# Kernel optimization log

Hardware: AMD Instinct MI355X
Metric: run time of the kernel (lower is better)

The kernel has to match this reference:

```python
import jax, jax.numpy as jnp
import numpy as np

INPUT_SIZE = 256
HIDDEN = 512

def setup_inputs() -> dict:
    key = jax.random.key(0)
    ks = jax.random.split(key, 12)
    B, T, I, H = 64, 1024, INPUT_SIZE, HIDDEN
    s = 1.0 / np.sqrt(I + H)
    x = jax.random.normal(ks[0], (B, T, I), dtype=jnp.float32)
    Wf = jax.random.uniform(ks[1], (I + H, H), jnp.float32, -s, s)
    bf = jax.random.uniform(ks[2], (H,), jnp.float32, -s, s)
    Wi = jax.random.uniform(ks[3], (I + H, H), jnp.float32, -s, s)
    bi = jax.random.uniform(ks[4], (H,), jnp.float32, -s, s)
    Wc = jax.random.uniform(ks[5], (I + H, H), jnp.float32, -s, s)
    bc = jax.random.uniform(ks[6], (H,), jnp.float32, -s, s)
    Wo = jax.random.uniform(ks[7], (I + H, H), jnp.float32, -s, s)
    bo = jax.random.uniform(ks[8], (H,), jnp.float32, -s, s)
    sf = 1.0 / np.sqrt(H)
    W_fc = jax.random.uniform(ks[9], (H, 1), jnp.float32, -sf, sf)
    b_fc = jax.random.uniform(ks[10], (1,), jnp.float32, -sf, sf)
    return {"x": x, "Wf": Wf, "bf": bf, "Wi": Wi, "bi": bi,
            "Wc": Wc, "bc": bc, "Wo": Wo, "bo": bo,
            "W_fc": W_fc, "b_fc": b_fc}

def reference(x, Wf, bf, Wi, bi, Wc, bc, Wo, bo, W_fc, b_fc):
    B, T, I = x.shape
    H = Wf.shape[1]
    # Fuse the 4 gate GEMMs into one [I+H, 4H] matmul (same math, one launch).
    W = jnp.concatenate([Wf, Wi, Wc, Wo], axis=1)   # [I+H, 4H]
    b = jnp.concatenate([bf, bi, bc, bo], axis=0)   # [4H]
    h0 = jnp.zeros((B, H), x.dtype)
    c0 = jnp.zeros((B, H), x.dtype)

    def step(carry, xt):
        h, c = carry
        combined = jnp.concatenate([xt, h], axis=1)     # [B, I+H]
        gates = combined @ W + b                        # [B, 4H]
        f, i, c_tilde, o = jnp.split(gates, 4, axis=1)
        f = jax.nn.sigmoid(f)
        i = jax.nn.sigmoid(i)
        c_tilde = jnp.tanh(c_tilde)
        o = jax.nn.sigmoid(o)
        c = f * c + i * c_tilde
        h = o * jnp.tanh(c)
        return (h, c), None

    (h, c), _ = jax.lax.scan(step, (h0, c0), jnp.swapaxes(x, 0, 1))
    return h @ W_fc + b_fc  # [B, 1]
```

## Files before the change

### kernel.cpp

```cpp
#include <hip/hip_runtime.h>
#include <hip/hip_fp16.h>


#define T_STEPS 1024
#define BATCH   64
#define ISZ     256
#define HSZ     512
#define NWG     128
#define NTHR    256
#define HB4     ((BATCH * HSZ) / 4)

typedef _Float16 half8  __attribute__((ext_vector_type(8)));
typedef _Float16 half4  __attribute__((ext_vector_type(4)));
typedef float    floatx4 __attribute__((ext_vector_type(4)));
typedef unsigned long long u64;

#define LD_AGENT(p)     __hip_atomic_load((p), __ATOMIC_RELAXED, __HIP_MEMORY_SCOPE_AGENT)
#define ST_AGENT(p, v)  __hip_atomic_store((p), (v), __ATOMIC_RELAXED, __HIP_MEMORY_SCOPE_AGENT)
#define ADD_AGENT(p, v) __hip_atomic_fetch_add((p), (v), __ATOMIC_RELAXED, __HIP_MEMORY_SCOPE_AGENT)

__device__ __forceinline__ float fast_sigmoid(float x) {
    return 1.0f / (1.0f + __expf(-x));
}
__device__ __forceinline__ float fast_tanh(float x) {
    return 1.0f - 2.0f / (__expf(2.0f * x) + 1.0f);
}

__global__ __launch_bounds__(NTHR, 1) void lstm_persist(
    const float* __restrict__ x,
    const float* __restrict__ Wf, const float* __restrict__ bfv,
    const float* __restrict__ Wi, const float* __restrict__ biv,
    const float* __restrict__ Wc, const float* __restrict__ bcv,
    const float* __restrict__ Wo, const float* __restrict__ bov,
    u64* __restrict__ hbuf4, unsigned* __restrict__ ctrs)
{
    const int g    = blockIdx.x;
    const int tid  = threadIdx.x;
    const int w    = tid >> 6;
    const int l    = tid & 63;
    const int lj   = l & 15;
    const int lk   = l >> 4;
    const int gate = lj >> 2;
    const int jc   = lj & 3;
    const int hc   = (g << 2) + jc;
    const int row0 = w << 4;
    const int arow = row0 + lj;
    const int grp  = g >> 3;

    const float* Wg = (gate == 0) ? Wf : (gate == 1) ? Wi : (gate == 2) ? Wc : Wo;
    const float* bg = (gate == 0) ? bfv : (gate == 1) ? biv : (gate == 2) ? bcv : bov;

    half8 Bfrag[24];
    #pragma unroll
    for (int kf = 0; kf < 24; ++kf) {
        half8 v;
        #pragma unroll
        for (int e = 0; e < 8; ++e) {
            int k = (kf << 5) + (lk << 3) + e;
            v[e] = (_Float16)Wg[(size_t)k * HSZ + hc];
        }
        Bfrag[kf] = v;
    }
    const float bias = bg[hc];
    float cst[4] = {0.f, 0.f, 0.f, 0.f};

    unsigned* lvl1 = &ctrs[grp * 16];
    unsigned* root = &ctrs[16 * 16];

    floatx4 accx = {0.f, 0.f, 0.f, 0.f};
    {
        const float* xr = x + (size_t)arow * T_STEPS * ISZ + (lk << 3);
        #pragma unroll
        for (int kf = 0; kf < 8; ++kf) {
            floatx4 x0 = *(const floatx4*)(xr + (kf << 5));
            floatx4 x1 = *(const floatx4*)(xr + (kf << 5) + 4);
            half8 a;
            a[0] = (_Float16)x0[0]; a[1] = (_Float16)x0[1];
            a[2] = (_Float16)x0[2]; a[3] = (_Float16)x0[3];
            a[4] = (_Float16)x1[0]; a[5] = (_Float16)x1[1];
            a[6] = (_Float16)x1[2]; a[7] = (_Float16)x1[3];
            accx = __builtin_amdgcn_mfma_f32_16x16x32_f16(a, Bfrag[kf], accx, 0, 0, 0);
        }
    }

    for (int t = 0; t < T_STEPS; ++t) {
        floatx4 acc;
        #pragma unroll
        for (int e = 0; e < 4; ++e) acc[e] = accx[e] + bias;

        if (t > 0) {
            if (tid == 0) {
                const unsigned tgt = 16u * (unsigned)t;
                while (LD_AGENT(root) < tgt) __builtin_amdgcn_s_sleep(1);
            }
            __syncthreads();

            const u64* hr = hbuf4 + (size_t)(t & 1) * HB4 + arow;
            u64 hl[32];
            #pragma unroll
            for (int kf = 0; kf < 16; ++kf) {
                const int c0 = kf * 8 + lk * 2;
                hl[2 * kf]     = LD_AGENT(hr + (size_t)c0 * BATCH);
                hl[2 * kf + 1] = LD_AGENT(hr + (size_t)(c0 + 1) * BATCH);
            }
            #pragma unroll
            for (int kf = 0; kf < 16; ++kf) {
                union { u64 u[2]; half8 h; } a;
                a.u[0] = hl[2 * kf];
                a.u[1] = hl[2 * kf + 1];
                acc = __builtin_amdgcn_mfma_f32_16x16x32_f16(a.h, Bfrag[8 + kf], acc, 0, 0, 0);
            }
        }

        floatx4 act;
        if (gate == 2) {
            #pragma unroll
            for (int e = 0; e < 4; ++e) act[e] = fast_tanh(acc[e]);
        } else {
            #pragma unroll
            for (int e = 0; e < 4; ++e) act[e] = fast_sigmoid(acc[e]);
        }

        const int base = l & ~12;
        float hv[4];
        #pragma unroll
        for (int e = 0; e < 4; ++e) {
            float vf = __shfl(act[e], base);
            float vi = __shfl(act[e], base + 4);
            float vc = __shfl(act[e], base + 8);
            float vo = __shfl(act[e], base + 12);
            float c  = vf * cst[e] + vi * vc;
            cst[e] = c;
            hv[e] = vo * fast_tanh(c);
        }

        half4 outv;
        #pragma unroll
        for (int col = 0; col < 4; ++col) {
            const int src = ((l & 15) >> 2) * 16 + col;
            float sel = 0.f;
            #pragma unroll
            for (int e = 0; e < 4; ++e) {
                float tmp = __shfl(hv[e], src);
                if ((l & 3) == e) sel = tmp;
            }
            outv[col] = (_Float16)sel;
        }
        u64* hw = hbuf4 + (size_t)((t + 1) & 1) * HB4 + (size_t)g * BATCH + row0;
        if (l < 16) {
            union { half4 h; u64 u; } pk; pk.h = outv;
            ST_AGENT(hw + l, pk.u);
        }
        asm volatile("s_waitcnt vmcnt(0)" ::: "memory");
        __syncthreads();

        if (tid == 0) {
            unsigned old = ADD_AGENT(lvl1, 1u);
            if (old == 8u * (unsigned)(t + 1) - 1u)
                ADD_AGENT(root, 1u);
        }

        if (t + 1 < T_STEPS) {
            floatx4 az = {0.f, 0.f, 0.f, 0.f};
            const float* xr = x + ((size_t)arow * T_STEPS + (t + 1)) * ISZ + (lk << 3);
            #pragma unroll
            for (int kf = 0; kf < 8; ++kf) {
                floatx4 x0 = *(const floatx4*)(xr + (kf << 5));
                floatx4 x1 = *(const floatx4*)(xr + (kf << 5) + 4);
                half8 a;
                a[0] = (_Float16)x0[0]; a[1] = (_Float16)x0[1];
                a[2] = (_Float16)x0[2]; a[3] = (_Float16)x0[3];
                a[4] = (_Float16)x1[0]; a[5] = (_Float16)x1[1];
                a[6] = (_Float16)x1[2]; a[7] = (_Float16)x1[3];
                az = __builtin_amdgcn_mfma_f32_16x16x32_f16(a, Bfrag[kf], az, 0, 0, 0);
            }
            accx = az;
        }
    }
}

__global__ void out_proj(const u64* __restrict__ hb4, const float* __restrict__ Wfc,
                         const float* __restrict__ bfc, float* __restrict__ out)
{
    const int b = blockIdx.x;
    const int l = threadIdx.x;
    float s = 0.f;
    #pragma unroll
    for (int j = 0; j < 2; ++j) {
        const int c4 = l + (j << 6);
        union { u64 u; half4 h; } v;
        v.u = hb4[(size_t)c4 * BATCH + b];
        #pragma unroll
        for (int q = 0; q < 4; ++q)
            s += (float)v.h[q] * Wfc[c4 * 4 + q];
    }
    #pragma unroll
    for (int off = 32; off; off >>= 1) s += __shfl_down(s, off);
    if (l == 0) out[b] = s + bfc[0];
}

extern "C" void kernel_launch(void* const* d_in, const int* in_sizes, int n_in,
                              void* d_out, int out_size, void* d_ws, size_t ws_size,
                              hipStream_t stream)
{
    const float* x   = (const float*)d_in[0];
    const float* Wf  = (const float*)d_in[1];
    const float* bf  = (const float*)d_in[2];
    const float* Wi  = (const float*)d_in[3];
    const float* bi  = (const float*)d_in[4];
    const float* Wc  = (const float*)d_in[5];
    const float* bc  = (const float*)d_in[6];
    const float* Wo  = (const float*)d_in[7];
    const float* bo  = (const float*)d_in[8];
    const float* Wfc = (const float*)d_in[9];
    const float* bfc = (const float*)d_in[10];

    u64* hbuf4 = (u64*)d_ws;
    unsigned* ctrs = (unsigned*)((char*)d_ws + 2 * HB4 * sizeof(u64));
    float* out = (float*)d_out;

    hipMemsetAsync(ctrs, 0, 2048, stream);

    void* args[] = { (void*)&x, (void*)&Wf, (void*)&bf, (void*)&Wi, (void*)&bi,
                     (void*)&Wc, (void*)&bc, (void*)&Wo, (void*)&bo,
                     (void*)&hbuf4, (void*)&ctrs };
    hipLaunchCooperativeKernel((void*)lstm_persist, dim3(NWG), dim3(NTHR),
                               args, 0, stream);

    out_proj<<<dim3(BATCH), dim3(64), 0, stream>>>(hbuf4, Wfc, bfc, (float*)d_out);
}
```

Baseline: 4.736 ms.

## Replace hierarchical atomic grid barrier with per-wave flag polling

Each wave now publishes its completed step in its own padded flag and waits only on the 128 flags of the waves that produce its batch rows, instead of a two-level atomic counter barrier followed by block-wide __syncthreads. This removes the serialized atomic chain and the intra-block syncs from the per-timestep critical path. The recurrent MFMA chain is also split into two independent accumulators to shorten its dependency latency. In exchange every wave polls 128 counters each step, which adds memory traffic and relies on relaxed-ordering visibility of the hidden-state stores before the flag store.

Measured after the change: 4.457 ms. 1.06x faster.

```diff
diff --git a/kernel.cpp b/kernel.cpp
--- a/kernel.cpp
+++ b/kernel.cpp
@@ -9,6 +9,7 @@
 #define NWG     128
 #define NTHR    256
 #define HB4     ((BATCH * HSZ) / 4)
+#define CTR_STRIDE 16
 
 typedef _Float16 half8  __attribute__((ext_vector_type(8)));
 typedef _Float16 half4  __attribute__((ext_vector_type(4)));
@@ -17,7 +18,6 @@
 
 #define LD_AGENT(p)     __hip_atomic_load((p), __ATOMIC_RELAXED, __HIP_MEMORY_SCOPE_AGENT)
 #define ST_AGENT(p, v)  __hip_atomic_store((p), (v), __ATOMIC_RELAXED, __HIP_MEMORY_SCOPE_AGENT)
-#define ADD_AGENT(p, v) __hip_atomic_fetch_add((p), (v), __ATOMIC_RELAXED, __HIP_MEMORY_SCOPE_AGENT)
 
 __device__ __forceinline__ float fast_sigmoid(float x) {
     return 1.0f / (1.0f + __expf(-x));
@@ -45,7 +45,6 @@
     const int hc   = (g << 2) + jc;
     const int row0 = w << 4;
     const int arow = row0 + lj;
-    const int grp  = g >> 3;
 
     const float* Wg = (gate == 0) ? Wf : (gate == 1) ? Wi : (gate == 2) ? Wc : Wo;
     const float* bg = (gate == 0) ? bfv : (gate == 1) ? biv : (gate == 2) ? bcv : bov;
@@ -64,8 +63,10 @@
     const float bias = bg[hc];
     float cst[4] = {0.f, 0.f, 0.f, 0.f};
 
-    unsigned* lvl1 = &ctrs[grp * 16];
-    unsigned* root = &ctrs[16 * 16];
+    unsigned* myctr = ctrs + ((size_t)w * NWG + g) * CTR_STRIDE;
+    const unsigned* cb = ctrs + (size_t)w * NWG * CTR_STRIDE;
+    const unsigned* cA = cb + (size_t)l * CTR_STRIDE;
+    const unsigned* cB = cb + (size_t)(l + 64) * CTR_STRIDE;
 
     floatx4 accx = {0.f, 0.f, 0.f, 0.f};
     {
@@ -84,16 +85,18 @@
     }
 
     for (int t = 0; t < T_STEPS; ++t) {
-        floatx4 acc;
-        #pragma unroll
-        for (int e = 0; e < 4; ++e) acc[e] = accx[e] + bias;
+        floatx4 acc0, acc1;
+        #pragma unroll
+        for (int e = 0; e < 4; ++e) { acc0[e] = accx[e] + bias; acc1[e] = 0.f; }
 
         if (t > 0) {
-            if (tid == 0) {
-                const unsigned tgt = 16u * (unsigned)t;
-                while (LD_AGENT(root) < tgt) __builtin_amdgcn_s_sleep(1);
-            }
-            __syncthreads();
+            const unsigned tgt = (unsigned)t;
+            while (true) {
+                unsigned a = LD_AGENT(cA);
+                unsigned b = LD_AGENT(cB);
+                if (__all((a >= tgt) && (b >= tgt))) break;
+                __builtin_amdgcn_s_sleep(1);
+            }
 
             const u64* hr = hbuf4 + (size_t)(t & 1) * HB4 + arow;
             u64 hl[32];
@@ -104,21 +107,22 @@
                 hl[2 * kf + 1] = LD_AGENT(hr + (size_t)(c0 + 1) * BATCH);
             }
             #pragma unroll
-            for (int kf = 0; kf < 16; ++kf) {
-                union { u64 u[2]; half8 h; } a;
-                a.u[0] = hl[2 * kf];
-                a.u[1] = hl[2 * kf + 1];
-                acc = __builtin_amdgcn_mfma_f32_16x16x32_f16(a.h, Bfrag[8 + kf], acc, 0, 0, 0);
+            for (int kf = 0; kf < 16; kf += 2) {
+                union { u64 u[2]; half8 h; } a0, a1;
+                a0.u[0] = hl[2 * kf];     a0.u[1] = hl[2 * kf + 1];
+                a1.u[0] = hl[2 * kf + 2]; a1.u[1] = hl[2 * kf + 3];
+                acc0 = __builtin_amdgcn_mfma_f32_16x16x32_f16(a0.h, Bfrag[8 + kf], acc0, 0, 0, 0);
+                acc1 = __builtin_amdgcn_mfma_f32_16x16x32_f16(a1.h, Bfrag[9 + kf], acc1, 0, 0, 0);
             }
         }
 
         floatx4 act;
         if (gate == 2) {
             #pragma unroll
-            for (int e = 0; e < 4; ++e) act[e] = fast_tanh(acc[e]);
+            for (int e = 0; e < 4; ++e) act[e] = fast_tanh(acc0[e] + acc1[e]);
         } else {
             #pragma unroll
-            for (int e = 0; e < 4; ++e) act[e] = fast_sigmoid(acc[e]);
+            for (int e = 0; e < 4; ++e) act[e] = fast_sigmoid(acc0[e] + acc1[e]);
         }
 
         const int base = l & ~12;
@@ -152,13 +156,7 @@
             ST_AGENT(hw + l, pk.u);
         }
         asm volatile("s_waitcnt vmcnt(0)" ::: "memory");
-        __syncthreads();
-
-        if (tid == 0) {
-            unsigned old = ADD_AGENT(lvl1, 1u);
-            if (old == 8u * (unsigned)(t + 1) - 1u)
-                ADD_AGENT(root, 1u);
-        }
+        if (l == 0) ST_AGENT(myctr, (unsigned)(t + 1));
 
         if (t + 1 < T_STEPS) {
             floatx4 az = {0.f, 0.f, 0.f, 0.f};
@@ -217,9 +215,8 @@
 
     u64* hbuf4 = (u64*)d_ws;
     unsigned* ctrs = (unsigned*)((char*)d_ws + 2 * HB4 * sizeof(u64));
-    float* out = (float*)d_out;
-
-    hipMemsetAsync(ctrs, 0, 2048, stream);
+
+    hipMemsetAsync(ctrs, 0, 4 * NWG * CTR_STRIDE * sizeof(unsigned), stream);
 
     void* args[] = { (void*)&x, (void*)&Wf, (void*)&bf, (void*)&Wi, (void*)&bi,
                      (void*)&Wc, (void*)&bc, (void*)&Wo, (void*)&bo,
```
